# Performance work log

Hardware: AMD Instinct MI355X
Metric: run time of the kernel (lower is better)

## Reference

```python
import jax, jax.numpy as jnp
import numpy as np

B, DIM, IN_DIM, H, W = 4, 512, 256, 64, 64
DOWN = IN_DIM // 2          # 128
QK = DOWN // 8              # 16
EPS = 1e-5


def conv2d(x, w, b, pad=0, dil=1):
    y = jax.lax.conv_general_dilated(
        x, w, window_strides=(1, 1),
        padding=[(pad, pad), (pad, pad)],
        rhs_dilation=(dil, dil),
        dimension_numbers=('NCHW', 'OIHW', 'NCHW'))
    return y + b[None, :, None, None]


def bn(x, g, bt, m, v):
    # inference-mode BatchNorm2d with running stats
    scale = (g * jax.lax.rsqrt(v + EPS))[None, :, None, None]
    return (x - m[None, :, None, None]) * scale + bt[None, :, None, None]


def prelu(x, a):
    return jnp.where(x >= 0, x, a * x)


def setup_inputs() -> dict:
    key = jax.random.key(0)
    ks = iter(jax.random.split(key, 64))
    d = {}
    d['x'] = jax.random.normal(next(ks), (B, DIM, H, W), dtype=jnp.float32)

    def conv_params(name, cout, cin, k):
        d[name + '_w'] = jax.random.normal(next(ks), (cout, cin, k, k), jnp.float32) * 0.05
        d[name + '_b'] = jax.random.normal(next(ks), (cout,), jnp.float32) * 0.05

    def bn_params(name, c):
        d[name + '_g'] = 1.0 + 0.1 * jax.random.normal(next(ks), (c,), jnp.float32)
        d[name + '_bt'] = 0.1 * jax.random.normal(next(ks), (c,), jnp.float32)
        d[name + '_m'] = 0.1 * jax.random.normal(next(ks), (c,), jnp.float32)
        d[name + '_v'] = 0.5 + jax.random.uniform(next(ks), (c,), jnp.float32)

    def prelu_param(name):
        d[name] = jnp.full((1,), 0.25, jnp.float32)

    conv_params('dc', IN_DIM, DIM, 3);  bn_params('dc_bn', IN_DIM); prelu_param('dc_a')
    conv_params('c1', DOWN, IN_DIM, 1); bn_params('c1_bn', DOWN);   prelu_param('c1_a')
    conv_params('c2', DOWN, IN_DIM, 3); bn_params('c2_bn', DOWN);   prelu_param('c2_a')
    conv_params('q', QK, DOWN, 1)
    conv_params('k', QK, DOWN, 1)
    conv_params('v', DOWN, DOWN, 1)
    d['gamma2'] = jnp.full((1,), 0.1, jnp.float32)  # torch init is 0; nonzero to exercise the path
    conv_params('c3', DOWN, IN_DIM, 1); bn_params('c3_bn', DOWN);   prelu_param('c3_a')
    conv_params('f', IN_DIM, 3 * DOWN, 1); bn_params('f_bn', IN_DIM); prelu_param('f_a')
    return d


def reference(x,
              dc_w, dc_b, dc_bn_g, dc_bn_bt, dc_bn_m, dc_bn_v, dc_a,
              c1_w, c1_b, c1_bn_g, c1_bn_bt, c1_bn_m, c1_bn_v, c1_a,
              c2_w, c2_b, c2_bn_g, c2_bn_bt, c2_bn_m, c2_bn_v, c2_a,
              q_w, q_b, k_w, k_b, v_w, v_b, gamma2,
              c3_w, c3_b, c3_bn_g, c3_bn_bt, c3_bn_m, c3_bn_v, c3_a,
              f_w, f_b, f_bn_g, f_bn_bt, f_bn_m, f_bn_v, f_a):
    # down_conv: 3x3 conv + BN + PReLU
    x = prelu(bn(conv2d(x, dc_w, dc_b, pad=1), dc_bn_g, dc_bn_bt, dc_bn_m, dc_bn_v), dc_a)
    # branch 1: 1x1 conv
    c1 = prelu(bn(conv2d(x, c1_w, c1_b), c1_bn_g, c1_bn_bt, c1_bn_m, c1_bn_v), c1_a)
    # branch 2: dilated 3x3 conv + non-local self-attention
    c2 = prelu(bn(conv2d(x, c2_w, c2_b, pad=2, dil=2), c2_bn_g, c2_bn_bt, c2_bn_m, c2_bn_v), c2_a)
    b, c, h, w = c2.shape
    hw = h * w
    q = conv2d(c2, q_w, q_b).reshape(b, QK, hw)   # [B, C/8, HW]
    k = conv2d(c2, k_w, k_b).reshape(b, QK, hw)
    v = conv2d(c2, v_w, v_b).reshape(b, c, hw)
    energy = jnp.einsum('bcn,bcm->bnm', q, k)     # [B, HW, HW]
    attn = jax.nn.softmax(energy, axis=-1)
    out2 = jnp.einsum('bcm,bnm->bcn', v, attn).reshape(b, c, h, w)
    out2 = gamma2 * out2 + c2
    # branch 3: global avg pool -> 1x1 conv -> broadcast (bilinear upsample of 1x1 is constant)
    pooled = jnp.mean(x, axis=(2, 3), keepdims=True)  # [B, IN_DIM, 1, 1]
    c3 = prelu(bn(conv2d(pooled, c3_w, c3_b), c3_bn_g, c3_bn_bt, c3_bn_m, c3_bn_v), c3_a)
    c3 = jnp.broadcast_to(c3, (b, DOWN, h, w))
    # fuse
    cat = jnp.concatenate([c1, out2, c3], axis=1)
    return prelu(bn(conv2d(cat, f_w, f_b), f_bn_g, f_bn_bt, f_bn_m, f_bn_v), f_a)
```

## Files before the change

kernel.cpp:

```cpp
#include <hip/hip_runtime.h>
#include <hip/hip_bf16.h>
#include <math.h>

#define HW 4096
#define EPSV 1e-5f

typedef unsigned short ushort;
typedef __attribute__((ext_vector_type(8))) short bf16x8;
typedef __attribute__((ext_vector_type(4))) float f32x4;

__device__ inline ushort f2bf(float f) {
    __hip_bfloat16 h = __float2bfloat16(f);
    return *reinterpret_cast<ushort*>(&h);
}
__device__ inline float bf2f(ushort u) {
    unsigned int v = ((unsigned int)u) << 16;
    return __uint_as_float(v);
}

__global__ __launch_bounds__(256) void pack_and_chlast(
    const float* __restrict__ dc_w, ushort* __restrict__ wdcp,
    const float* __restrict__ c2_w, ushort* __restrict__ wc2p,
    const float* __restrict__ c1_w, ushort* __restrict__ wc1b,
    const float* __restrict__ f_w,  ushort* __restrict__ wfb,
    float* __restrict__ pool,
    const float* __restrict__ x, ushort* __restrict__ xbf)
{
    constexpr int PACK_BLKS = 6148;
    constexpr int T_DC = 9 * 16 * 256 * 32;
    constexpr int T_C2 = 9 * 8 * 128 * 32;
    constexpr int T_C1 = 32768;
    constexpr int T_F  = 65536;
    const int tid = threadIdx.x;
    __shared__ float sT[64][65];

    if (blockIdx.x < PACK_BLKS) {
        int idx = blockIdx.x * 256 + tid;
        if (idx < T_DC) {
            const int ci_in = idx & 31;
            int rest = idx >> 5;
            const int co = rest % 256; rest /= 256;
            const int cc = rest % 16;
            const int tap = rest / 16;
            wdcp[idx] = f2bf(dc_w[((size_t)co * 512 + cc * 32 + ci_in) * 9 + tap]);
            return;
        }
        idx -= T_DC;
        if (idx < T_C2) {
            const int ci_in = idx & 31;
            int rest = idx >> 5;
            const int co = rest % 128; rest /= 128;
            const int cc = rest % 8;
            const int tap = rest / 8;
            wc2p[idx] = f2bf(c2_w[((size_t)co * 256 + cc * 32 + ci_in) * 9 + tap]);
            return;
        }
        idx -= T_C2;
        if (idx < T_C1) { wc1b[idx] = f2bf(c1_w[idx]); return; }
        idx -= T_C1;
        if (idx < T_F) {
            const int co = idx >> 8, k = idx & 255;
            wfb[idx] = f2bf(f_w[co * 384 + k]);
            return;
        }
        idx -= T_F;
        if (idx < 1024) pool[idx] = 0.f;
        return;
    }

    const int f = blockIdx.x - PACK_BLKS;
    const int p0 = (f & 63) * 64;
    const int c0 = ((f >> 6) & 7) * 64;
    const int b  = f >> 9;
    for (int i = tid; i < 4096; i += 256) {
        const int ch = i >> 6, px = i & 63;
        sT[ch][px] = x[(size_t)(b * 512 + c0 + ch) * HW + p0 + px];
    }
    __syncthreads();
    const int px = tid >> 2, seg = tid & 3;
    ushort tmp[16];
    #pragma unroll
    for (int j = 0; j < 16; ++j) tmp[j] = f2bf(sT[seg * 16 + j][px]);
    ushort* d = xbf + (size_t)(b * HW + p0 + px) * 512 + c0 + seg * 16;
    *(uint4*)d = *(uint4*)&tmp[0];
    *(uint4*)(d + 8) = *(uint4*)&tmp[8];
}

template<int CIN, int COUT, int COTILE, int DIL, int ROWS, int OMODE>
__global__ __launch_bounds__(256, OMODE == 0 ? 4 : 2) void conv3x3_fused(
    const ushort* __restrict__ xin,
    const ushort* __restrict__ wpk,
    const float* __restrict__ bias, const float* __restrict__ bng,
    const float* __restrict__ bnb, const float* __restrict__ bnm,
    const float* __restrict__ bnv, const float* __restrict__ al,
    void* __restrict__ outv,
    float* __restrict__ pool)
{
    constexpr int HR = ROWS + 2 * DIL;
    constexpr int NC = 64 + 2 * DIL;
    constexpr int MT = COTILE / 16;
    constexpr int WPR = 4 / ROWS;
    constexpr int NT = ROWS;
    constexpr int SAS = 40;
    constexpr int CH = CIN / 32;
    constexpr int NA = HR * NC * 4;
    constexpr int NREG = (NA + 255) / 256;
    constexpr int WCH = 9 * MT * 64;
    constexpr int WPT = (WCH + 255) / 256;

    const int tid = threadIdx.x;
    const int wave = tid >> 6, lane = tid & 63;
    const int l15 = lane & 15, quad = lane >> 4;
    const int b = blockIdx.z;
    const int cob = blockIdx.y;
    const int co0 = cob * COTILE;
    const int h0 = blockIdx.x * ROWS;
    const int row = wave / WPR;
    const int ntbase = (wave % WPR) * NT;

    __shared__ __align__(16) ushort sA[HR * NC * SAS];
    __shared__ __align__(16) ushort sW[WCH * 8];

    f32x4 acc[MT][NT];
    #pragma unroll
    for (int mt = 0; mt < MT; ++mt)
        #pragma unroll
        for (int nt = 0; nt < NT; ++nt) acc[mt][nt] = (f32x4){0.f, 0.f, 0.f, 0.f};

    #pragma unroll 1
    for (int cc = 0; cc < CH; ++cc) {
        if (cc != 0) __syncthreads();
        #pragma unroll
        for (int k = 0; k < NREG; ++k) {
            const int i = tid + k * 256;
            if (i < NA) {
                const int p = i >> 2, seg = i & 3;
                const int r = p / NC, c = p - r * NC;
                const int grow = h0 - DIL + r, gcol = c - DIL;
                uint4 val = {0u, 0u, 0u, 0u};
                if (grow >= 0 && grow < 64 && gcol >= 0 && gcol < 64)
                    val = *(const uint4*)&xin[((size_t)(b * 64 + grow) * 64 + gcol) * CIN
                                              + cc * 32 + seg * 8];
                *(uint4*)&sA[p * SAS + seg * 8] = val;
            }
        }
        #pragma unroll
        for (int k = 0; k < WPT; ++k) {
            const int i = tid + k * 256;
            if (i < WCH) {
                const int tap = i / (MT * 64);
                const int r = i - tap * (MT * 64);
                const int mt = r >> 6, n = r & 63;
                const uint4 wv = *(const uint4*)&wpk[
                    ((size_t)(tap * (CIN / 32) + cc) * COUT + co0 + mt * 16 + (n & 15)) * 32
                    + (n >> 4) * 8];
                *(uint4*)&sW[i * 8] = wv;
            }
        }
        __syncthreads();

        #pragma unroll
        for (int tap = 0; tap < 9; ++tap) {
            const int ty = tap / 3, tx = tap - ty * 3;
            const int rl = row + ty * DIL;
            bf16x8 wf[MT];
            #pragma unroll
            for (int mt = 0; mt < MT; ++mt)
                wf[mt] = *(const bf16x8*)&sW[((tap * MT + mt) * 64 + lane) * 8];
            #pragma unroll
            for (int nt = 0; nt < NT; ++nt) {
                const int cl = (ntbase + nt) * 16 + l15 + tx * DIL;
                const bf16x8 bp = *(const bf16x8*)&sA[(rl * NC + cl) * SAS + quad * 8];
                #pragma unroll
                for (int mt = 0; mt < MT; ++mt)
                    acc[mt][nt] = __builtin_amdgcn_mfma_f32_16x16x32_bf16(
                        wf[mt], bp, acc[mt][nt], 0, 0, 0);
            }
        }
    }

    const float a = al[0];

    if constexpr (OMODE == 0) {
        __syncthreads();
        ushort* sT = sA;
        #pragma unroll
        for (int mt = 0; mt < MT; ++mt) {
            float sc[4], sh[4], psum[4];
            #pragma unroll
            for (int rr = 0; rr < 4; ++rr) {
                const int co = co0 + mt * 16 + quad * 4 + rr;
                sc[rr] = bng[co] * rsqrtf(bnv[co] + EPSV);
                sh[rr] = (bias[co] - bnm[co]) * sc[rr] + bnb[co];
                psum[rr] = 0.f;
            }
            #pragma unroll
            for (int nt = 0; nt < NT; ++nt) {
                float tv[4];
                #pragma unroll
                for (int rr = 0; rr < 4; ++rr) {
                    float t = acc[mt][nt][rr] * sc[rr] + sh[rr];
                    t = t >= 0.f ? t : a * t;
                    tv[rr] = t;
                    psum[rr] += t;
                }
                ushort4 u;
                u.x = f2bf(tv[0]); u.y = f2bf(tv[1]);
                u.z = f2bf(tv[2]); u.w = f2bf(tv[3]);
                const int px = (ntbase + nt) * 16 + l15;
                *(ushort4*)&sT[(row * 64 + px) * 40 + mt * 16 + quad * 4] = u;
            }
            #pragma unroll
            for (int rr = 0; rr < 4; ++rr) {
                float v = psum[rr];
                v += __shfl_xor(v, 1);
                v += __shfl_xor(v, 2);
                v += __shfl_xor(v, 4);
                v += __shfl_xor(v, 8);
                if (l15 == 0)
                    atomicAdd(&pool[b * 256 + co0 + mt * 16 + quad * 4 + rr], v);
            }
        }
        __syncthreads();
        ushort* dst = (ushort*)outv;
        const int p = tid >> 1, half = tid & 1;
        const uint4 v0 = *(const uint4*)&sT[p * 40 + half * 16];
        const uint4 v1 = *(const uint4*)&sT[p * 40 + half * 16 + 8];
        const size_t off = ((size_t)(b * 4096 + (h0 + (p >> 6)) * 64 + (p & 63))) * 256
                           + co0 + half * 16;
        *(uint4*)&dst[off] = v0;
        *(uint4*)&dst[off + 8] = v1;
    } else {
        float* out = (float*)outv;
        #pragma unroll
        for (int mt = 0; mt < MT; ++mt)
            #pragma unroll
            for (int rr = 0; rr < 4; ++rr) {
                const int co = co0 + mt * 16 + quad * 4 + rr;
                const float sc = bng[co] * rsqrtf(bnv[co] + EPSV);
                const float sh = (bias[co] - bnm[co]) * sc + bnb[co];
                #pragma unroll
                for (int nt = 0; nt < NT; ++nt) {
                    float t = acc[mt][nt][rr] * sc + sh;
                    t = t >= 0.f ? t : a * t;
                    out[((size_t)(b * COUT + co) * 64 + h0 + row) * 64
                        + (ntbase + nt) * 16 + l15] = t;
                }
            }
    }
}

__global__ __launch_bounds__(256, 2) void c2_c1_c3(
    const ushort* __restrict__ xin,
    const ushort* __restrict__ wpk,
    const float* __restrict__ c2bias, const float* __restrict__ c2gn,
    const float* __restrict__ c2bt, const float* __restrict__ c2mn,
    const float* __restrict__ c2vr, const float* __restrict__ c2al,
    float* __restrict__ c2out,
    const ushort* __restrict__ wbf,
    const float* __restrict__ bias, const float* __restrict__ bng,
    const float* __restrict__ bnb, const float* __restrict__ bnm,
    const float* __restrict__ bnv, const float* __restrict__ al,
    ushort* __restrict__ catb,
    const float* __restrict__ pool, const float* __restrict__ c3w,
    const float* __restrict__ c3b, const float* __restrict__ c3g,
    const float* __restrict__ c3bt, const float* __restrict__ c3m,
    const float* __restrict__ c3v, const float* __restrict__ c3a,
    const float* __restrict__ fw, float* __restrict__ fbias)
{
    const int tid = threadIdx.x;
    const int wave = tid >> 6, lane = tid & 63;
    const int l15 = lane & 15, quad = lane >> 4;
    __shared__ __align__(16) char smem[51072];

    if (blockIdx.x < 32) {
        constexpr int CIN = 256, COUT = 128, COTILE = 32, DIL = 2, ROWS = 2;
        constexpr int HR = ROWS + 2 * DIL;
        constexpr int NC = 64 + 2 * DIL;
        constexpr int MT = COTILE / 16;
        constexpr int WPR = 4 / ROWS;
        constexpr int NT = ROWS;
        constexpr int SAS = 40;
        constexpr int CH = CIN / 32;
        constexpr int NA = HR * NC * 4;
        constexpr int NREG = (NA + 255) / 256;
        constexpr int WCH = 9 * MT * 64;
        constexpr int WPT = (WCH + 255) / 256;

        ushort* sA = (ushort*)smem;
        ushort* sW = (ushort*)(smem + 32640);

        const int b = blockIdx.z;
        const int co0 = blockIdx.y * COTILE;
        const int h0 = blockIdx.x * ROWS;
        const int row = wave / WPR;
        const int ntbase = (wave % WPR) * NT;

        f32x4 acc[MT][NT];
        #pragma unroll
        for (int mt = 0; mt < MT; ++mt)
            #pragma unroll
            for (int nt = 0; nt < NT; ++nt) acc[mt][nt] = (f32x4){0.f, 0.f, 0.f, 0.f};

        #pragma unroll 1
        for (int cc = 0; cc < CH; ++cc) {
            if (cc != 0) __syncthreads();
            #pragma unroll
            for (int k = 0; k < NREG; ++k) {
                const int i = tid + k * 256;
                if (i < NA) {
                    const int p = i >> 2, seg = i & 3;
                    const int r = p / NC, c = p - r * NC;
                    const int grow = h0 - DIL + r, gcol = c - DIL;
                    uint4 val = {0u, 0u, 0u, 0u};
                    if (grow >= 0 && grow < 64 && gcol >= 0 && gcol < 64)
                        val = *(const uint4*)&xin[((size_t)(b * 64 + grow) * 64 + gcol) * CIN
                                                  + cc * 32 + seg * 8];
                    *(uint4*)&sA[p * SAS + seg * 8] = val;
                }
            }
            #pragma unroll
            for (int k = 0; k < WPT; ++k) {
                const int i = tid + k * 256;
                if (i < WCH) {
                    const int tap = i / (MT * 64);
                    const int r = i - tap * (MT * 64);
                    const int mt = r >> 6, n = r & 63;
                    const uint4 wv = *(const uint4*)&wpk[
                        ((size_t)(tap * (CIN / 32) + cc) * COUT + co0 + mt * 16 + (n & 15)) * 32
                        + (n >> 4) * 8];
                    *(uint4*)&sW[i * 8] = wv;
                }
            }
            __syncthreads();

            #pragma unroll
            for (int tap = 0; tap < 9; ++tap) {
                const int ty = tap / 3, tx = tap - ty * 3;
                const int rl = row + ty * DIL;
                bf16x8 wf[MT];
                #pragma unroll
                for (int mt = 0; mt < MT; ++mt)
                    wf[mt] = *(const bf16x8*)&sW[((tap * MT + mt) * 64 + lane) * 8];
                #pragma unroll
                for (int nt = 0; nt < NT; ++nt) {
                    const int cl = (ntbase + nt) * 16 + l15 + tx * DIL;
                    const bf16x8 bp = *(const bf16x8*)&sA[(rl * NC + cl) * SAS + quad * 8];
                    #pragma unroll
                    for (int mt = 0; mt < MT; ++mt)
                        acc[mt][nt] = __builtin_amdgcn_mfma_f32_16x16x32_bf16(
                            wf[mt], bp, acc[mt][nt], 0, 0, 0);
                }
            }
        }

        const float a = c2al[0];
        #pragma unroll
        for (int mt = 0; mt < MT; ++mt)
            #pragma unroll
            for (int rr = 0; rr < 4; ++rr) {
                const int co = co0 + mt * 16 + quad * 4 + rr;
                const float sc = c2gn[co] * rsqrtf(c2vr[co] + EPSV);
                const float sh = (c2bias[co] - c2mn[co]) * sc + c2bt[co];
                #pragma unroll
                for (int nt = 0; nt < NT; ++nt) {
                    float t = acc[mt][nt][rr] * sc + sh;
                    t = t >= 0.f ? t : a * t;
                    c2out[((size_t)(b * COUT + co) * 64 + h0 + row) * 64
                          + (ntbase + nt) * 16 + l15] = t;
                }
            }
        return;
    }

    const int flat = (blockIdx.z * 4 + blockIdx.y) * 17 + (blockIdx.x - 32);
    if (flat >= 260) return;
    const int bx = flat % 130, by = flat / 130;

    if (bx >= 128) {
        const int b = (bx - 128) * 2 + by;
        float* sp  = (float*)smem;
        float* sc3 = (float*)(smem + 2048);
        sp[tid] = pool[b * 256 + tid] * (1.0f / 4096.0f);
        __syncthreads();
        if (tid < 128) {
            float acc2 = c3b[tid];
            for (int ci = 0; ci < 256; ++ci) acc2 = fmaf(c3w[tid * 256 + ci], sp[ci], acc2);
            const float scale = c3g[tid] * rsqrtf(c3v[tid] + EPSV);
            float t = (acc2 - c3m[tid]) * scale + c3bt[tid];
            const float a2 = c3a[0];
            sc3[tid] = t >= 0.f ? t : a2 * t;
        }
        __syncthreads();
        float f = 0.f;
        for (int j2 = 0; j2 < 128; ++j2) f = fmaf(fw[tid * 384 + 256 + j2], sc3[j2], f);
        fbias[b * 256 + tid] = f;
        return;
    }

    {
        constexpr int CIN = 256;
        const int pix0 = bx * 128 + wave * 32;
        const int co0 = by * 64;

        f32x4 acc[4][2];
        #pragma unroll
        for (int mt = 0; mt < 4; ++mt)
            #pragma unroll
            for (int nt = 0; nt < 2; ++nt) acc[mt][nt] = (f32x4){0.f, 0.f, 0.f, 0.f};

        #pragma unroll 2
        for (int cc = 0; cc < CIN / 32; ++cc) {
            bf16x8 aw[4], bp[2];
            #pragma unroll
            for (int mt = 0; mt < 4; ++mt)
                aw[mt] = *(const bf16x8*)&wbf[(size_t)(co0 + mt * 16 + l15) * CIN + cc * 32 + quad * 8];
            #pragma unroll
            for (int nt = 0; nt < 2; ++nt)
                bp[nt] = *(const bf16x8*)&xin[(size_t)(pix0 + nt * 16 + l15) * CIN + cc * 32 + quad * 8];
            #pragma unroll
            for (int mt = 0; mt < 4; ++mt)
                #pragma unroll
                for (int nt = 0; nt < 2; ++nt)
                    acc[mt][nt] = __builtin_amdgcn_mfma_f32_16x16x32_bf16(
                        aw[mt], bp[nt], acc[mt][nt], 0, 0, 0);
        }

        const float a = al[0];
        ushort* sT = (ushort*)smem;
        #pragma unroll
        for (int mt = 0; mt < 4; ++mt)
            #pragma unroll
            for (int r = 0; r < 4; ++r) {
                const int co = co0 + mt * 16 + quad * 4 + r;
                const float scale = bng[co] * rsqrtf(bnv[co] + EPSV);
                const float shift = bias[co] * scale + (bnb[co] - bnm[co] * scale);
                #pragma unroll
                for (int nt = 0; nt < 2; ++nt) {
                    float t = acc[mt][nt][r] * scale + shift;
                    t = t >= 0.f ? t : a * t;
                    sT[((wave * 32 + nt * 16 + l15) * 68) + mt * 16 + quad * 4 + r] = f2bf(t);
                }
            }
        __syncthreads();
        const int p = lane >> 1, half = lane & 1;
        #pragma unroll
        for (int seg = 0; seg < 4; ++seg) {
            uint2 a0 = *(uint2*)&sT[((wave * 32 + p) * 68) + half * 32 + seg * 8];
            uint2 a1 = *(uint2*)&sT[((wave * 32 + p) * 68) + half * 32 + seg * 8 + 4];
            uint4 vv = {a0.x, a0.y, a1.x, a1.y};
            *(uint4*)&catb[(size_t)(pix0 + p) * 256 + co0 + half * 32 + seg * 8] = vv;
        }
    }
}

template<int CIN, int COUT, bool BNACT, int OMODE>
__global__ __launch_bounds__(256) void gemm1x1_cl(
    const ushort* __restrict__ xin,
    const ushort* __restrict__ wbf,
    const float* __restrict__ bias, const float* __restrict__ bng,
    const float* __restrict__ bnb, const float* __restrict__ bnm,
    const float* __restrict__ bnv, const float* __restrict__ al,
    const float* __restrict__ ebias, void* __restrict__ outv,
    int ostride, int ocol)
{
    const int tid = threadIdx.x;
    const int wave = tid >> 6, lane = tid & 63;
    const int l15 = lane & 15, quad = lane >> 4;
    const int pix0 = blockIdx.x * 128 + wave * 32;
    const int co0 = blockIdx.y * 64;

    f32x4 acc[4][2];
    #pragma unroll
    for (int mt = 0; mt < 4; ++mt)
        #pragma unroll
        for (int nt = 0; nt < 2; ++nt) acc[mt][nt] = (f32x4){0.f, 0.f, 0.f, 0.f};

    #pragma unroll 2
    for (int cc = 0; cc < CIN / 32; ++cc) {
        bf16x8 aw[4], bp[2];
        #pragma unroll
        for (int mt = 0; mt < 4; ++mt)
            aw[mt] = *(const bf16x8*)&wbf[(size_t)(co0 + mt * 16 + l15) * CIN + cc * 32 + quad * 8];
        #pragma unroll
        for (int nt = 0; nt < 2; ++nt)
            bp[nt] = *(const bf16x8*)&xin[(size_t)(pix0 + nt * 16 + l15) * CIN + cc * 32 + quad * 8];
        #pragma unroll
        for (int mt = 0; mt < 4; ++mt)
            #pragma unroll
            for (int nt = 0; nt < 2; ++nt)
                acc[mt][nt] = __builtin_amdgcn_mfma_f32_16x16x32_bf16(
                    aw[mt], bp[nt], acc[mt][nt], 0, 0, 0);
    }

    const int bI = pix0 >> 12;
    const float a = BNACT ? al[0] : 0.f;

    if (OMODE == 0) {
        float* out = (float*)outv;
        #pragma unroll
        for (int mt = 0; mt < 4; ++mt)
            #pragma unroll
            for (int r = 0; r < 4; ++r) {
                const int co = co0 + mt * 16 + quad * 4 + r;
                float bb = bias[co];
                if (ebias) bb += ebias[bI * COUT + co];
                float scale = 1.f, shift = bb;
                if (BNACT) {
                    scale = bng[co] * rsqrtf(bnv[co] + EPSV);
                    shift = bb * scale + (bnb[co] - bnm[co] * scale);
                }
                #pragma unroll
                for (int nt = 0; nt < 2; ++nt) {
                    float t = acc[mt][nt][r] * scale + shift;
                    if (BNACT) t = t >= 0.f ? t : a * t;
                    out[((size_t)(bI * COUT + co)) * HW + (pix0 & 4095) + nt * 16 + l15] = t;
                }
            }
    } else {
        __shared__ ushort sT[4][32][68];
        #pragma unroll
        for (int mt = 0; mt < 4; ++mt)
            #pragma unroll
            for (int r = 0; r < 4; ++r) {
                const int co = co0 + mt * 16 + quad * 4 + r;
                float bb = bias[co];
                float scale = 1.f, shift = bb;
                if (BNACT) {
                    scale = bng[co] * rsqrtf(bnv[co] + EPSV);
                    shift = bb * scale + (bnb[co] - bnm[co] * scale);
                }
                #pragma unroll
                for (int nt = 0; nt < 2; ++nt) {
                    float t = acc[mt][nt][r] * scale + shift;
                    if (BNACT) t = t >= 0.f ? t : a * t;
                    sT[wave][nt * 16 + l15][mt * 16 + quad * 4 + r] = f2bf(t);
                }
            }
        __syncthreads();
        const int p = lane >> 1, half = lane & 1;
        ushort* out = (ushort*)outv;
        #pragma unroll
        for (int seg = 0; seg < 4; ++seg) {
            uint2 a0 = *(uint2*)&sT[wave][p][half * 32 + seg * 8];
            uint2 a1 = *(uint2*)&sT[wave][p][half * 32 + seg * 8 + 4];
            uint4 vv = {a0.x, a0.y, a1.x, a1.y};
            *(uint4*)&out[(size_t)(pix0 + p) * ostride + ocol + co0 + half * 32 + seg * 8] = vv;
        }
    }
}

__global__ __launch_bounds__(256) void qkv_kernel(
    const float* __restrict__ c2g, const float* __restrict__ qw,
    const float* __restrict__ qb2, const float* __restrict__ kw,
    const float* __restrict__ kb2, ushort* __restrict__ qpack,
    ushort* __restrict__ kpack,
    const float* __restrict__ vw, const float* __restrict__ vb,
    ushort* __restrict__ vbh)
{
    const int tid = threadIdx.x;
    const int b = blockIdx.z, p0 = blockIdx.x * 64;
    __shared__ __align__(16) char smem[49152];

    if (blockIdx.y == 0) {
        float (*sC)[64]   = (float(*)[64])smem;
        float (*sWq)[128] = (float(*)[128])(smem + 32768);
        float (*sWk)[128] = (float(*)[128])(smem + 40960);
        for (int i = tid; i < 8192; i += 256) {
            const int px = i & 63, ci = i >> 6;
            sC[ci][px] = c2g[(size_t)(b * 128 + ci) * HW + p0 + px];
        }
        for (int i = tid; i < 2048; i += 256) {
            const int ci = i & 127, co = i >> 7;
            sWq[co][ci] = qw[co * 128 + ci];
            sWk[co][ci] = kw[co * 128 + ci];
        }
        __syncthreads();
        const int px = tid & 63, grp = tid >> 6;
        const int co0 = (grp & 1) * 8;
        const bool isK = grp >= 2;
        const float* sWp = isK ? &sWk[0][0] : &sWq[0][0];
        float acc[8] = {};
        for (int ci = 0; ci < 128; ++ci) {
            const float xv = sC[ci][px];
            #pragma unroll
            for (int j = 0; j < 8; ++j)
                acc[j] = fmaf(sWp[(co0 + j) * 128 + ci], xv, acc[j]);
        }
        const float* bsrc = isK ? kb2 : qb2;
        ushort* osrc = isK ? kpack : qpack;
        const size_t base = (size_t)(b * 4096 + p0 + px) * 32;
        #pragma unroll
        for (int j = 0; j < 8; ++j) {
            osrc[base + co0 + j] = f2bf(acc[j] + bsrc[co0 + j]);
            osrc[base + 16 + co0 + j] = 0;
        }
    } else {
        const int co0 = (blockIdx.y - 1) * 64;
        float* sIn = (float*)smem;
        float* sW  = (float*)(smem + 16384);
        const int cg = tid >> 4, pg = tid & 15;
        const int c0l = cg * 4, w0 = pg * 4;
        float acc[4][4] = {};
        for (int cc = 0; cc < 128; cc += 16) {
            {
                int i = tid;
                #pragma unroll
                for (int it = 0; it < 4; ++it, i += 256) {
                    const int px = i & 63, ci = i >> 6;
                    sIn[ci * 64 + px] = c2g[(size_t)(b * 128 + cc + ci) * HW + p0 + px];
                }
                i = tid;
                #pragma unroll
                for (int it = 0; it < 4; ++it, i += 256) {
                    const int ci = i & 15, co = i >> 4;
                    sW[ci * 68 + co] = vw[(co0 + co) * 128 + cc + ci];
                }
            }
            __syncthreads();
            #pragma unroll
            for (int ci = 0; ci < 16; ++ci) {
                const float4 iv = *(const float4*)&sIn[ci * 64 + w0];
                const float4 wv = *(const float4*)&sW[ci * 68 + c0l];
                const float ia[4] = {iv.x, iv.y, iv.z, iv.w};
                const float wa[4] = {wv.x, wv.y, wv.z, wv.w};
                #pragma unroll
                for (int i2 = 0; i2 < 4; ++i2)
                    #pragma unroll
                    for (int j = 0; j < 4; ++j)
                        acc[i2][j] = fmaf(wa[i2], ia[j], acc[i2][j]);
            }
            __syncthreads();
        }
        #pragma unroll
        for (int i2 = 0; i2 < 4; ++i2) {
            const int co = co0 + c0l + i2;
            const float shift = vb[co];
            const size_t base = (size_t)(b * 128 + co) * HW + p0 + w0;
            #pragma unroll
            for (int j = 0; j < 4; ++j)
                vbh[base + j] = f2bf(acc[i2][j] + shift);
        }
    }
}

__global__ __launch_bounds__(256) void attn_flash(
    const ushort* __restrict__ qpack,
    const ushort* __restrict__ kpack,
    const ushort* __restrict__ vpackT,
    ushort* __restrict__ opart,
    float* __restrict__ Mpart,
    float* __restrict__ Spart)
{
    const int tid = threadIdx.x;
    const int wave = tid >> 6, lane = tid & 63;
    const int l15 = lane & 15, quad = lane >> 4;
    const int b = blockIdx.z, j = blockIdx.y;
    const int n0w = blockIdx.x * 128 + wave * 32;
    const int m_begin = j * 512;

    __shared__ __align__(16) ushort sV[2][128][40];
    __shared__ __align__(16) ushort sP[4][2][16][40];

    const bf16x8 bq0 = *(const bf16x8*)(qpack + ((size_t)(b * 4096 + n0w + l15) * 32 + quad * 8));
    const bf16x8 bq1 = *(const bf16x8*)(qpack + ((size_t)(b * 4096 + n0w + 16 + l15) * 32 + quad * 8));
    const f32x4 z = {0.f, 0.f, 0.f, 0.f};

    float runM0 = -3e30f, runM1 = -3e30f;
    float runS0 = 0.f, runS1 = 0.f;
    f32x4 oacc0[8], oacc1[8];
    #pragma unroll
    for (int cs = 0; cs < 8; ++cs) {
        oacc0[cs] = (f32x4){0.f, 0.f, 0.f, 0.f};
        oacc1[cs] = (f32x4){0.f, 0.f, 0.f, 0.f};
    }

    const int stc = tid >> 1, stseg = tid & 1;

    {
        uint4 v0 = *(const uint4*)&vpackT[(size_t)(b * 128 + stc) * HW + m_begin + stseg * 16];
        uint4 v1 = *(const uint4*)&vpackT[(size_t)(b * 128 + stc) * HW + m_begin + stseg * 16 + 8];
        *(uint4*)&sV[0][stc][stseg * 16] = v0;
        *(uint4*)&sV[0][stc][stseg * 16 + 8] = v1;
    }
    __syncthreads();

    #pragma unroll 1
    for (int t = 0; t < 16; ++t) {
        const int m0 = m_begin + t * 32;
        const int buf = t & 1;
        uint4 nv0, nv1;
        const bool more = (t + 1 < 16);
        if (more) {
            const size_t nb = (size_t)(b * 128 + stc) * HW + m0 + 32 + stseg * 16;
            nv0 = *(const uint4*)&vpackT[nb];
            nv1 = *(const uint4*)&vpackT[nb + 8];
        }
        f32x4 s0[2], s1[2];
        #pragma unroll
        for (int ms = 0; ms < 2; ++ms) {
            const bf16x8 ak = *(const bf16x8*)(
                kpack + ((size_t)(b * 4096 + m0 + ms * 16 + l15) * 32 + quad * 8));
            s0[ms] = __builtin_amdgcn_mfma_f32_16x16x32_bf16(ak, bq0, z, 0, 0, 0);
            s1[ms] = __builtin_amdgcn_mfma_f32_16x16x32_bf16(ak, bq1, z, 0, 0, 0);
        }

        float tM0 = fmaxf(fmaxf(fmaxf(s0[0][0], s0[0][1]), fmaxf(s0[0][2], s0[0][3])),
                          fmaxf(fmaxf(s0[1][0], s0[1][1]), fmaxf(s0[1][2], s0[1][3])));
        float tM1 = fmaxf(fmaxf(fmaxf(s1[0][0], s1[0][1]), fmaxf(s1[0][2], s1[0][3])),
                          fmaxf(fmaxf(s1[1][0], s1[1][1]), fmaxf(s1[1][2], s1[1][3])));
        tM0 = fmaxf(tM0, __shfl_xor(tM0, 16));
        tM0 = fmaxf(tM0, __shfl_xor(tM0, 32));
        tM1 = fmaxf(tM1, __shfl_xor(tM1, 16));
        tM1 = fmaxf(tM1, __shfl_xor(tM1, 32));
        if (__any(tM0 > runM0 + 8.f)) {
            const float nM = fmaxf(runM0, tM0);
            const float sc = __builtin_amdgcn_exp2f((runM0 - nM) * 1.44269504f);
            runS0 *= sc;
            float scr[4];
            #pragma unroll
            for (int r = 0; r < 4; ++r) scr[r] = __shfl(sc, quad * 4 + r);
            #pragma unroll
            for (int cs = 0; cs < 8; ++cs) {
                oacc0[cs][0] *= scr[0]; oacc0[cs][1] *= scr[1];
                oacc0[cs][2] *= scr[2]; oacc0[cs][3] *= scr[3];
            }
            runM0 = nM;
        }
        if (__any(tM1 > runM1 + 8.f)) {
            const float nM = fmaxf(runM1, tM1);
            const float sc = __builtin_amdgcn_exp2f((runM1 - nM) * 1.44269504f);
            runS1 *= sc;
            float scr[4];
            #pragma unroll
            for (int r = 0; r < 4; ++r) scr[r] = __shfl(sc, quad * 4 + r);
            #pragma unroll
            for (int cs = 0; cs < 8; ++cs) {
                oacc1[cs][0] *= scr[0]; oacc1[cs][1] *= scr[1];
                oacc1[cs][2] *= scr[2]; oacc1[cs][3] *= scr[3];
            }
            runM1 = nM;
        }
        const float Ms0 = runM0 * 1.44269504f;
        const float Ms1 = runM1 * 1.44269504f;

        #pragma unroll
        for (int ms = 0; ms < 2; ++ms) {
            float p0[4], p1[4];
            #pragma unroll
            for (int r = 0; r < 4; ++r) {
                p0[r] = __builtin_amdgcn_exp2f(fmaf(s0[ms][r], 1.44269504f, -Ms0));
                p1[r] = __builtin_amdgcn_exp2f(fmaf(s1[ms][r], 1.44269504f, -Ms1));
                runS0 += p0[r];
                runS1 += p1[r];
            }
            ushort4 u0, u1;
            u0.x = f2bf(p0[0]); u0.y = f2bf(p0[1]); u0.z = f2bf(p0[2]); u0.w = f2bf(p0[3]);
            u1.x = f2bf(p1[0]); u1.y = f2bf(p1[1]); u1.z = f2bf(p1[2]); u1.w = f2bf(p1[3]);
            *(uint2*)&sP[wave][0][l15][ms * 16 + quad * 4] = *(uint2*)&u0;
            *(uint2*)&sP[wave][1][l15][ms * 16 + quad * 4] = *(uint2*)&u1;
        }
        asm volatile("s_waitcnt lgkmcnt(0)" ::: "memory");
        const bf16x8 ap0 = *(const bf16x8*)&sP[wave][0][l15][quad * 8];
        const bf16x8 ap1 = *(const bf16x8*)&sP[wave][1][l15][quad * 8];
        #pragma unroll
        for (int cs = 0; cs < 8; ++cs) {
            const bf16x8 bv = *(const bf16x8*)&sV[buf][cs * 16 + l15][quad * 8];
            oacc0[cs] = __builtin_amdgcn_mfma_f32_16x16x32_bf16(ap0, bv, oacc0[cs], 0, 0, 0);
            oacc1[cs] = __builtin_amdgcn_mfma_f32_16x16x32_bf16(ap1, bv, oacc1[cs], 0, 0, 0);
        }
        if (more) {
            *(uint4*)&sV[buf ^ 1][stc][stseg * 16] = nv0;
            *(uint4*)&sV[buf ^ 1][stc][stseg * 16 + 8] = nv1;
            __syncthreads();
        }
    }

    runS0 += __shfl_xor(runS0, 16);
    runS0 += __shfl_xor(runS0, 32);
    runS1 += __shfl_xor(runS1, 16);
    runS1 += __shfl_xor(runS1, 32);
    if (lane < 32) {
        const float Mv = (lane < 16) ? runM0 : runM1;
        const float Sv = (lane < 16) ? runS0 : runS1;
        const int n = n0w + ((lane < 16) ? 0 : 16) + l15;
        Mpart[((size_t)b * 8 + j) * 4096 + n] = Mv;
        Spart[((size_t)b * 8 + j) * 4096 + n] = Sv;
    }
    #pragma unroll
    for (int cs = 0; cs < 8; ++cs)
        #pragma unroll
        for (int r = 0; r < 4; ++r) {
            const int n = n0w + quad * 4 + r;
            opart[(((size_t)b * 8 + j) * 4096 + n) * 128 + cs * 16 + l15] = f2bf(oacc0[cs][r]);
            opart[(((size_t)b * 8 + j) * 4096 + n + 16) * 128 + cs * 16 + l15] = f2bf(oacc1[cs][r]);
        }
}

__global__ __launch_bounds__(256) void attn_combine(
    const ushort* __restrict__ opart, const float* __restrict__ Mpart,
    const float* __restrict__ Spart, const float* __restrict__ c2g,
    const float* __restrict__ gamma2, ushort* __restrict__ catb)
{
    const int b = blockIdx.y, n0 = blockIdx.x * 32, tid = threadIdx.x;
    __shared__ float sC2[128][33];
    __shared__ float sWj[8][32];
    if (tid < 32) {
        const int n = n0 + tid;
        float Mj[8], Sj[8];
        #pragma unroll
        for (int j = 0; j < 8; ++j) {
            Mj[j] = Mpart[((size_t)b * 8 + j) * 4096 + n];
            Sj[j] = Spart[((size_t)b * 8 + j) * 4096 + n];
        }
        float M = -3e30f;
        #pragma unroll
        for (int j = 0; j < 8; ++j) M = fmaxf(M, Mj[j]);
        float St = 0.f, e[8];
        #pragma unroll
        for (int j = 0; j < 8; ++j) { e[j] = __expf(Mj[j] - M); St += Sj[j] * e[j]; }
        const float inv = 1.0f / St;
        #pragma unroll
        for (int j = 0; j < 8; ++j) sWj[j][tid] = e[j] * inv;
    }
    #pragma unroll
    for (int e = 0; e < 16; ++e) {
        const int idx = tid + e * 256;
        const int c = idx >> 5, n = idx & 31;
        sC2[c][n] = c2g[(size_t)(b * 128 + c) * HW + n0 + n];
    }
    __syncthreads();
    const float g2 = gamma2[0];
    #pragma unroll
    for (int e = 0; e < 16; ++e) {
        const int idx = tid + e * 256;
        const int n = idx >> 7, c = idx & 127;
        float s = 0.f;
        #pragma unroll
        for (int j = 0; j < 8; ++j)
            s += bf2f(opart[(((size_t)b * 8 + j) * 4096 + n0 + n) * 128 + c]) * sWj[j][n];
        catb[(size_t)(b * 4096 + n0 + n) * 256 + 128 + c] = f2bf(fmaf(g2, s, sC2[c][n]));
    }
}

extern "C" void kernel_launch(void* const* d_in, const int* in_sizes, int n_in,
                              void* d_out, int out_size, void* d_ws, size_t ws_size,
                              hipStream_t stream)
{
    const float* x     = (const float*)d_in[0];
    const float* dc_w  = (const float*)d_in[1];
    const float* dc_b  = (const float*)d_in[2];
    const float* dc_g  = (const float*)d_in[3];
    const float* dc_bt = (const float*)d_in[4];
    const float* dc_m  = (const float*)d_in[5];
    const float* dc_v  = (const float*)d_in[6];
    const float* dc_a  = (const float*)d_in[7];
    const float* c1_w  = (const float*)d_in[8];
    const float* c1_b  = (const float*)d_in[9];
    const float* c1_g  = (const float*)d_in[10];
    const float* c1_bt = (const float*)d_in[11];
    const float* c1_m  = (const float*)d_in[12];
    const float* c1_v  = (const float*)d_in[13];
    const float* c1_a  = (const float*)d_in[14];
    const float* c2_w  = (const float*)d_in[15];
    const float* c2_b  = (const float*)d_in[16];
    const float* c2_g  = (const float*)d_in[17];
    const float* c2_bt = (const float*)d_in[18];
    const float* c2_m  = (const float*)d_in[19];
    const float* c2_v  = (const float*)d_in[20];
    const float* c2_a  = (const float*)d_in[21];
    const float* q_w   = (const float*)d_in[22];
    const float* q_b   = (const float*)d_in[23];
    const float* k_w   = (const float*)d_in[24];
    const float* k_b   = (const float*)d_in[25];
    const float* v_w   = (const float*)d_in[26];
    const float* v_b   = (const float*)d_in[27];
    const float* gamma2= (const float*)d_in[28];
    const float* c3_w  = (const float*)d_in[29];
    const float* c3_b  = (const float*)d_in[30];
    const float* c3_g  = (const float*)d_in[31];
    const float* c3_bt = (const float*)d_in[32];
    const float* c3_m  = (const float*)d_in[33];
    const float* c3_v  = (const float*)d_in[34];
    const float* c3_a  = (const float*)d_in[35];
    const float* f_w   = (const float*)d_in[36];
    const float* f_b   = (const float*)d_in[37];
    const float* f_g   = (const float*)d_in[38];
    const float* f_bt  = (const float*)d_in[39];
    const float* f_m   = (const float*)d_in[40];
    const float* f_v   = (const float*)d_in[41];
    const float* f_a   = (const float*)d_in[42];

    char* base = (char*)d_ws;
    ushort* xbf   = (ushort*)base;
    ushort* opart = (ushort*)base;
    ushort* qpk   = (ushort*)(base + 33554432);
    ushort* kpk   = (ushort*)(base + 34603008);
    ushort* vbh   = (ushort*)(base + 35651584);
    float*  c2b   = (float*)(base + 39845888);
    ushort* xpbf  = (ushort*)(base + 50331648);
    ushort* catb  = (ushort*)(base + 58720256);
    ushort* wdcp  = (ushort*)(base + 75497472);
    ushort* wc2p  = (ushort*)(base + 77856768);
    ushort* wc1b  = (ushort*)(base + 78446592);
    ushort* wfb   = (ushort*)(base + 78512128);
    float*  poolb = (float*)(base + 78643200);
    float*  fbb   = (float*)(base + 78647296);
    float*  Mpart = (float*)(base + 78651392);
    float*  Spart = (float*)(base + 79175680);

    pack_and_chlast<<<dim3(6148 + 2048), 256, 0, stream>>>(
        dc_w, wdcp, c2_w, wc2p, c1_w, wc1b, f_w, wfb, poolb, x, xbf);
    conv3x3_fused<512, 256, 32, 1, 2, 0><<<dim3(32, 8, 4), 256, 0, stream>>>(
        xbf, wdcp, dc_b, dc_g, dc_bt, dc_m, dc_v, dc_a, xpbf, poolb);
    c2_c1_c3<<<dim3(49, 4, 4), 256, 0, stream>>>(
        xpbf, wc2p, c2_b, c2_g, c2_bt, c2_m, c2_v, c2_a, c2b,
        wc1b, c1_b, c1_g, c1_bt, c1_m, c1_v, c1_a, catb,
        poolb, c3_w, c3_b, c3_g, c3_bt, c3_m, c3_v, c3_a, f_w, fbb);
    qkv_kernel<<<dim3(64, 3, 4), 256, 0, stream>>>(
        c2b, q_w, q_b, k_w, k_b, qpk, kpk, v_w, v_b, vbh);
    attn_flash<<<dim3(32, 8, 4), 256, 0, stream>>>(qpk, kpk, vbh, opart, Mpart, Spart);
    attn_combine<<<dim3(128, 4), 256, 0, stream>>>(opart, Mpart, Spart, c2b, gamma2, catb);
    gemm1x1_cl<256, 256, true, 0><<<dim3(128, 4), 256, 0, stream>>>(
        catb, wfb, f_b, f_g, f_bt, f_m, f_v, f_a, fbb, (float*)d_out, 0, 0);
}
```

Measured before the change: 374.4 us.

## Store c2 as channel-last bf16 and compute QKV projections with MFMA

The c2 branch output is now written as channel-last bf16 through a shared-memory transpose, where it used to be NCHW fp32. The q/k/v 1x1 projections are rewritten to read this layout and run as bf16 MFMA tiles, using weights pre-packed to bf16 in the pack kernel. attn_combine is adapted to read the bf16 channel-last c2. This reduces c2 memory traffic and replaces scalar FMA loops with matrix-core work, at the cost of extra bf16 rounding on c2 and on the projection weights.

```diff
diff --git a/kernel.cpp b/kernel.cpp
--- a/kernel.cpp
+++ b/kernel.cpp
@@ -23,14 +23,19 @@
     const float* __restrict__ c2_w, ushort* __restrict__ wc2p,
     const float* __restrict__ c1_w, ushort* __restrict__ wc1b,
     const float* __restrict__ f_w,  ushort* __restrict__ wfb,
+    const float* __restrict__ q_w,  const float* __restrict__ k_w,
+    ushort* __restrict__ wqkb,
+    const float* __restrict__ v_w,  ushort* __restrict__ wvb,
     float* __restrict__ pool,
     const float* __restrict__ x, ushort* __restrict__ xbf)
 {
-    constexpr int PACK_BLKS = 6148;
+    constexpr int PACK_BLKS = 6228;
     constexpr int T_DC = 9 * 16 * 256 * 32;
     constexpr int T_C2 = 9 * 8 * 128 * 32;
     constexpr int T_C1 = 32768;
     constexpr int T_F  = 65536;
+    constexpr int T_QK = 4096;
+    constexpr int T_V  = 16384;
     const int tid = threadIdx.x;
     __shared__ float sT[64][65];
 
@@ -64,6 +69,13 @@
             return;
         }
         idx -= T_F;
+        if (idx < T_QK) {
+            wqkb[idx] = f2bf(idx < 2048 ? q_w[idx] : k_w[idx - 2048]);
+            return;
+        }
+        idx -= T_QK;
+        if (idx < T_V) { wvb[idx] = f2bf(v_w[idx]); return; }
+        idx -= T_V;
         if (idx < 1024) pool[idx] = 0.f;
         return;
     }
@@ -256,7 +268,7 @@
     const float* __restrict__ c2bias, const float* __restrict__ c2gn,
     const float* __restrict__ c2bt, const float* __restrict__ c2mn,
     const float* __restrict__ c2vr, const float* __restrict__ c2al,
-    float* __restrict__ c2out,
+    ushort* __restrict__ c2out,
     const ushort* __restrict__ wbf,
     const float* __restrict__ bias, const float* __restrict__ bng,
     const float* __restrict__ bnb, const float* __restrict__ bnm,
@@ -355,21 +367,40 @@
         }
 
         const float a = c2al[0];
-        #pragma unroll
-        for (int mt = 0; mt < MT; ++mt)
+        __syncthreads();
+        ushort* sTc = (ushort*)smem;
+        #pragma unroll
+        for (int mt = 0; mt < MT; ++mt) {
+            float sc[4], sh[4];
             #pragma unroll
             for (int rr = 0; rr < 4; ++rr) {
                 const int co = co0 + mt * 16 + quad * 4 + rr;
-                const float sc = c2gn[co] * rsqrtf(c2vr[co] + EPSV);
-                const float sh = (c2bias[co] - c2mn[co]) * sc + c2bt[co];
-                #pragma unroll
-                for (int nt = 0; nt < NT; ++nt) {
-                    float t = acc[mt][nt][rr] * sc + sh;
-                    t = t >= 0.f ? t : a * t;
-                    c2out[((size_t)(b * COUT + co) * 64 + h0 + row) * 64
-                          + (ntbase + nt) * 16 + l15] = t;
-                }
-            }
+                sc[rr] = c2gn[co] * rsqrtf(c2vr[co] + EPSV);
+                sh[rr] = (c2bias[co] - c2mn[co]) * sc[rr] + c2bt[co];
+            }
+            #pragma unroll
+            for (int nt = 0; nt < NT; ++nt) {
+                float tv[4];
+                #pragma unroll
+                for (int rr = 0; rr < 4; ++rr) {
+                    float t = acc[mt][nt][rr] * sc[rr] + sh[rr];
+                    tv[rr] = t >= 0.f ? t : a * t;
+                }
+                ushort4 u;
+                u.x = f2bf(tv[0]); u.y = f2bf(tv[1]);
+                u.z = f2bf(tv[2]); u.w = f2bf(tv[3]);
+                const int px = (ntbase + nt) * 16 + l15;
+                *(ushort4*)&sTc[(row * 64 + px) * 40 + mt * 16 + quad * 4] = u;
+            }
+        }
+        __syncthreads();
+        const int p = tid >> 1, half = tid & 1;
+        const uint4 v0 = *(const uint4*)&sTc[p * 40 + half * 16];
+        const uint4 v1 = *(const uint4*)&sTc[p * 40 + half * 16 + 8];
+        const size_t off = ((size_t)(b * 4096 + (h0 + (p >> 6)) * 64 + (p & 63))) * 128
+                           + co0 + half * 16;
+        *(uint4*)&c2out[off] = v0;
+        *(uint4*)&c2out[off + 8] = v1;
         return;
     }
 
@@ -550,97 +581,99 @@
     }
 }
 
-__global__ __launch_bounds__(256) void qkv_kernel(
-    const float* __restrict__ c2g, const float* __restrict__ qw,
-    const float* __restrict__ qb2, const float* __restrict__ kw,
-    const float* __restrict__ kb2, ushort* __restrict__ qpack,
-    ushort* __restrict__ kpack,
-    const float* __restrict__ vw, const float* __restrict__ vb,
-    ushort* __restrict__ vbh)
+__global__ __launch_bounds__(256) void qkv_mfma(
+    const ushort* __restrict__ c2bh,
+    const ushort* __restrict__ wqkb,
+    const float* __restrict__ qb2, const float* __restrict__ kb2,
+    ushort* __restrict__ qpack, ushort* __restrict__ kpack,
+    const ushort* __restrict__ wvb,
+    const float* __restrict__ vb, ushort* __restrict__ vbh)
 {
     const int tid = threadIdx.x;
-    const int b = blockIdx.z, p0 = blockIdx.x * 64;
-    __shared__ __align__(16) char smem[49152];
+    const int wave = tid >> 6, lane = tid & 63;
+    const int l15 = lane & 15, quad = lane >> 4;
+    const int b = blockIdx.z;
+    const int pix0 = blockIdx.x * 128 + wave * 32;
+    const size_t xrow = (size_t)(b * 4096);
 
     if (blockIdx.y == 0) {
-        float (*sC)[64]   = (float(*)[64])smem;
-        float (*sWq)[128] = (float(*)[128])(smem + 32768);
-        float (*sWk)[128] = (float(*)[128])(smem + 40960);
-        for (int i = tid; i < 8192; i += 256) {
-            const int px = i & 63, ci = i >> 6;
-            sC[ci][px] = c2g[(size_t)(b * 128 + ci) * HW + p0 + px];
-        }
-        for (int i = tid; i < 2048; i += 256) {
-            const int ci = i & 127, co = i >> 7;
-            sWq[co][ci] = qw[co * 128 + ci];
-            sWk[co][ci] = kw[co * 128 + ci];
-        }
+        f32x4 acc[2][2];
+        #pragma unroll
+        for (int mt = 0; mt < 2; ++mt)
+            #pragma unroll
+            for (int nt = 0; nt < 2; ++nt) acc[mt][nt] = (f32x4){0.f, 0.f, 0.f, 0.f};
+        #pragma unroll
+        for (int cc = 0; cc < 4; ++cc) {
+            bf16x8 aw[2], bp[2];
+            #pragma unroll
+            for (int mt = 0; mt < 2; ++mt)
+                aw[mt] = *(const bf16x8*)&wqkb[(mt * 16 + l15) * 128 + cc * 32 + quad * 8];
+            #pragma unroll
+            for (int nt = 0; nt < 2; ++nt)
+                bp[nt] = *(const bf16x8*)&c2bh[(xrow + pix0 + nt * 16 + l15) * 128 + cc * 32 + quad * 8];
+            #pragma unroll
+            for (int mt = 0; mt < 2; ++mt)
+                #pragma unroll
+                for (int nt = 0; nt < 2; ++nt)
+                    acc[mt][nt] = __builtin_amdgcn_mfma_f32_16x16x32_bf16(
+                        aw[mt], bp[nt], acc[mt][nt], 0, 0, 0);
+        }
+        __shared__ __align__(16) ushort sT[4][32][40];
+        #pragma unroll
+        for (int mt = 0; mt < 2; ++mt)
+            #pragma unroll
+            for (int r = 0; r < 4; ++r) {
+                const int co = mt * 16 + quad * 4 + r;
+                const float bb = (co < 16) ? qb2[co] : kb2[co - 16];
+                #pragma unroll
+                for (int nt = 0; nt < 2; ++nt)
+                    sT[wave][nt * 16 + l15][co] = f2bf(acc[mt][nt][r] + bb);
+            }
         __syncthreads();
-        const int px = tid & 63, grp = tid >> 6;
-        const int co0 = (grp & 1) * 8;
-        const bool isK = grp >= 2;
-        const float* sWp = isK ? &sWk[0][0] : &sWq[0][0];
-        float acc[8] = {};
-        for (int ci = 0; ci < 128; ++ci) {
-            const float xv = sC[ci][px];
-            #pragma unroll
-            for (int j = 0; j < 8; ++j)
-                acc[j] = fmaf(sWp[(co0 + j) * 128 + ci], xv, acc[j]);
-        }
-        const float* bsrc = isK ? kb2 : qb2;
-        ushort* osrc = isK ? kpack : qpack;
-        const size_t base = (size_t)(b * 4096 + p0 + px) * 32;
-        #pragma unroll
-        for (int j = 0; j < 8; ++j) {
-            osrc[base + co0 + j] = f2bf(acc[j] + bsrc[co0 + j]);
-            osrc[base + 16 + co0 + j] = 0;
-        }
+        const int p = lane >> 1, half = lane & 1;
+        ushort* dst = half ? kpack : qpack;
+        const int cbase = half ? 16 : 0;
+        const size_t off = (size_t)(b * 4096 + pix0 + p) * 32;
+        *(uint4*)&dst[off]     = *(uint4*)&sT[wave][p][cbase];
+        *(uint4*)&dst[off + 8] = *(uint4*)&sT[wave][p][cbase + 8];
+        const uint4 zz = {0u, 0u, 0u, 0u};
+        *(uint4*)&dst[off + 16] = zz;
+        *(uint4*)&dst[off + 24] = zz;
     } else {
         const int co0 = (blockIdx.y - 1) * 64;
-        float* sIn = (float*)smem;
-        float* sW  = (float*)(smem + 16384);
-        const int cg = tid >> 4, pg = tid & 15;
-        const int c0l = cg * 4, w0 = pg * 4;
-        float acc[4][4] = {};
-        for (int cc = 0; cc < 128; cc += 16) {
-            {
-                int i = tid;
-                #pragma unroll
-                for (int it = 0; it < 4; ++it, i += 256) {
-                    const int px = i & 63, ci = i >> 6;
-                    sIn[ci * 64 + px] = c2g[(size_t)(b * 128 + cc + ci) * HW + p0 + px];
-                }
-                i = tid;
-                #pragma unroll
-                for (int it = 0; it < 4; ++it, i += 256) {
-                    const int ci = i & 15, co = i >> 4;
-                    sW[ci * 68 + co] = vw[(co0 + co) * 128 + cc + ci];
-                }
-            }
-            __syncthreads();
-            #pragma unroll
-            for (int ci = 0; ci < 16; ++ci) {
-                const float4 iv = *(const float4*)&sIn[ci * 64 + w0];
-                const float4 wv = *(const float4*)&sW[ci * 68 + c0l];
-                const float ia[4] = {iv.x, iv.y, iv.z, iv.w};
-                const float wa[4] = {wv.x, wv.y, wv.z, wv.w};
-                #pragma unroll
-                for (int i2 = 0; i2 < 4; ++i2)
-                    #pragma unroll
-                    for (int j = 0; j < 4; ++j)
-                        acc[i2][j] = fmaf(wa[i2], ia[j], acc[i2][j]);
-            }
-            __syncthreads();
-        }
-        #pragma unroll
-        for (int i2 = 0; i2 < 4; ++i2) {
-            const int co = co0 + c0l + i2;
-            const float shift = vb[co];
-            const size_t base = (size_t)(b * 128 + co) * HW + p0 + w0;
-            #pragma unroll
-            for (int j = 0; j < 4; ++j)
-                vbh[base + j] = f2bf(acc[i2][j] + shift);
-        }
+        f32x4 acc[4][2];
+        #pragma unroll
+        for (int mt = 0; mt < 4; ++mt)
+            #pragma unroll
+            for (int nt = 0; nt < 2; ++nt) acc[mt][nt] = (f32x4){0.f, 0.f, 0.f, 0.f};
+        #pragma unroll
+        for (int cc = 0; cc < 4; ++cc) {
+            bf16x8 aw[4], bp[2];
+            #pragma unroll
+            for (int mt = 0; mt < 4; ++mt)
+                aw[mt] = *(const bf16x8*)&wvb[(size_t)(co0 + mt * 16 + l15) * 128 + cc * 32 + quad * 8];
+            #pragma unroll
+            for (int nt = 0; nt < 2; ++nt)
+                bp[nt] = *(const bf16x8*)&c2bh[(xrow + pix0 + nt * 16 + l15) * 128 + cc * 32 + quad * 8];
+            #pragma unroll
+            for (int mt = 0; mt < 4; ++mt)
+                #pragma unroll
+                for (int nt = 0; nt < 2; ++nt)
+                    acc[mt][nt] = __builtin_amdgcn_mfma_f32_16x16x32_bf16(
+                        aw[mt], bp[nt], acc[mt][nt], 0, 0, 0);
+        }
+        #pragma unroll
+        for (int mt = 0; mt < 4; ++mt)
+            #pragma unroll
+            for (int r = 0; r < 4; ++r) {
+                const int co = co0 + mt * 16 + quad * 4 + r;
+                const float shift = vb[co];
+                #pragma unroll
+                for (int nt = 0; nt < 2; ++nt) {
+                    const int px = pix0 + nt * 16 + l15;
+                    vbh[(size_t)(b * 128 + co) * HW + px] = f2bf(acc[mt][nt][r] + shift);
+                }
+            }
     }
 }
 
@@ -799,7 +832,7 @@
 
 __global__ __launch_bounds__(256) void attn_combine(
     const ushort* __restrict__ opart, const float* __restrict__ Mpart,
-    const float* __restrict__ Spart, const float* __restrict__ c2g,
+    const float* __restrict__ Spart, const ushort* __restrict__ c2bh,
     const float* __restrict__ gamma2, ushort* __restrict__ catb)
 {
     const int b = blockIdx.y, n0 = blockIdx.x * 32, tid = threadIdx.x;
@@ -826,8 +859,8 @@
     #pragma unroll
     for (int e = 0; e < 16; ++e) {
         const int idx = tid + e * 256;
-        const int c = idx >> 5, n = idx & 31;
-        sC2[c][n] = c2g[(size_t)(b * 128 + c) * HW + n0 + n];
+        const int n = idx >> 7, c = idx & 127;
+        sC2[c][n] = bf2f(c2bh[(size_t)(b * 4096 + n0 + n) * 128 + c]);
     }
     __syncthreads();
     const float g2 = gamma2[0];
@@ -897,7 +930,9 @@
     ushort* qpk   = (ushort*)(base + 33554432);
     ushort* kpk   = (ushort*)(base + 34603008);
     ushort* vbh   = (ushort*)(base + 35651584);
-    float*  c2b   = (float*)(base + 39845888);
+    ushort* c2bh  = (ushort*)(base + 39845888);
+    ushort* wqkb  = (ushort*)(base + 48234496);
+    ushort* wvb   = (ushort*)(base + 48242688);
     ushort* xpbf  = (ushort*)(base + 50331648);
     ushort* catb  = (ushort*)(base + 58720256);
     ushort* wdcp  = (ushort*)(base + 75497472);
@@ -909,18 +944,19 @@
     float*  Mpart = (float*)(base + 78651392);
     float*  Spart = (float*)(base + 79175680);
 
-    pack_and_chlast<<<dim3(6148 + 2048), 256, 0, stream>>>(
-        dc_w, wdcp, c2_w, wc2p, c1_w, wc1b, f_w, wfb, poolb, x, xbf);
+    pack_and_chlast<<<dim3(6228 + 2048), 256, 0, stream>>>(
+        dc_w, wdcp, c2_w, wc2p, c1_w, wc1b, f_w, wfb,
+        q_w, k_w, wqkb, v_w, wvb, poolb, x, xbf);
     conv3x3_fused<512, 256, 32, 1, 2, 0><<<dim3(32, 8, 4), 256, 0, stream>>>(
         xbf, wdcp, dc_b, dc_g, dc_bt, dc_m, dc_v, dc_a, xpbf, poolb);
     c2_c1_c3<<<dim3(49, 4, 4), 256, 0, stream>>>(
-        xpbf, wc2p, c2_b, c2_g, c2_bt, c2_m, c2_v, c2_a, c2b,
+        xpbf, wc2p, c2_b, c2_g, c2_bt, c2_m, c2_v, c2_a, c2bh,
         wc1b, c1_b, c1_g, c1_bt, c1_m, c1_v, c1_a, catb,
         poolb, c3_w, c3_b, c3_g, c3_bt, c3_m, c3_v, c3_a, f_w, fbb);
-    qkv_kernel<<<dim3(64, 3, 4), 256, 0, stream>>>(
-        c2b, q_w, q_b, k_w, k_b, qpk, kpk, v_w, v_b, vbh);
+    qkv_mfma<<<dim3(32, 3, 4), 256, 0, stream>>>(
+        c2bh, wqkb, q_b, k_b, qpk, kpk, wvb, v_b, vbh);
     attn_flash<<<dim3(32, 8, 4), 256, 0, stream>>>(qpk, kpk, vbh, opart, Mpart, Spart);
-    attn_combine<<<dim3(128, 4), 256, 0, stream>>>(opart, Mpart, Spart, c2b, gamma2, catb);
+    attn_combine<<<dim3(128, 4), 256, 0, stream>>>(opart, Mpart, Spart, c2bh, gamma2, catb);
     gemm1x1_cl<256, 256, true, 0><<<dim3(128, 4), 256, 0, stream>>>(
         catb, wfb, f_b, f_g, f_bt, f_m, f_v, f_a, fbb, (float*)d_out, 0, 0);
 }
```

New measurement: 369.0 us. About the same (-1.4%).
